# Kernel optimization log

Hardware: AMD Instinct MI355X
Metric: run time of the kernel (lower is better)

## Reference

```python
import jax, jax.numpy as jnp
import numpy as np
import math

B, S, DM, H = 2, 2048, 1024, 16
HD = DM // H  # head_dim = 64


def setup_inputs() -> dict:
    key = jax.random.key(0)
    ks = jax.random.split(key, 7)
    mk = lambda k, shp, s=1.0: jax.random.normal(k, shp, dtype=jnp.float32) * s
    return {
        "q": mk(ks[0], (B, S, DM)),
        "k": mk(ks[1], (B, S, DM)),
        "v": mk(ks[2], (B, S, DM)),
        "wq": mk(ks[3], (DM, DM), 0.02),
        "wk": mk(ks[4], (DM, DM), 0.02),
        "wv": mk(ks[5], (DM, DM), 0.02),
        "wo": mk(ks[6], (DM, DM), 0.02),
    }


def reference(q, k, v, wq, wk, wv, wo):
    bsz, seqlen, _ = q.shape
    # bias-free linear projections: y = x @ W.T (torch nn.Linear layout [out,in])
    def proj(x, w):
        y = jnp.einsum('bsd,ed->bse', x, w)
        return y.reshape(bsz, seqlen, H, HD).transpose(0, 2, 1, 3)  # (B,H,S,HD)
    xq, xk, xv = proj(q, wq), proj(k, wk), proj(v, wv)
    scores = jnp.einsum('bhqd,bhkd->bhqk', xq, xk) / math.sqrt(HD)  # (B,H,S,S)
    # causal mask: -inf above the diagonal
    causal = jnp.tril(jnp.ones((seqlen, seqlen), dtype=bool))
    scores = jnp.where(causal[None, None], scores, -jnp.inf)
    probs = jax.nn.softmax(scores.astype(jnp.float32), axis=-1).astype(xq.dtype)
    # dropout p=0.0 -> identity in eval / p=0 config
    out = jnp.einsum('bhqk,bhkd->bhqd', probs, xv)  # (B,H,S,HD)
    out = out.transpose(0, 2, 1, 3).reshape(bsz, seqlen, DM)
    return jnp.einsum('bsd,ed->bse', out, wo)
```

## Files before the change

kernel.cpp:

```cpp
#include <hip/hip_runtime.h>
#include <hip/hip_bf16.h>
#include <stdint.h>

#define NB 2
#define NS 2048
#define NDM 1024
#define NH 16
#define NHD 64
#define NTOK (NB * NS)

typedef __bf16 bf16x8 __attribute__((ext_vector_type(8)));
typedef float f32x4 __attribute__((ext_vector_type(4)));
typedef uint16_t u16x8 __attribute__((ext_vector_type(8)));

static __device__ __forceinline__ uint16_t f2bf(float f) {
  __bf16 b = (__bf16)f;
  union { __bf16 b; uint16_t u; } x; x.b = b;
  return x.u;
}

static __device__ __forceinline__ u16x8 cvt8(float4 a, float4 b) {
  u16x8 v;
  v[0] = f2bf(a.x); v[1] = f2bf(a.y); v[2] = f2bf(a.z); v[3] = f2bf(a.w);
  v[4] = f2bf(b.x); v[5] = f2bf(b.y); v[6] = f2bf(b.z); v[7] = f2bf(b.w);
  return v;
}

static __device__ __forceinline__ void gload_lds16(const void* g, void* l) {
  __builtin_amdgcn_global_load_lds(
      (const __attribute__((address_space(1))) void*)g,
      (__attribute__((address_space(3))) void*)l, 16, 0, 0);
}

__global__ __launch_bounds__(256) void cvt_w(
    const float* __restrict__ w0, const float* __restrict__ w1,
    const float* __restrict__ w2, const float* __restrict__ w3,
    uint16_t* __restrict__ o0, uint16_t* __restrict__ o1,
    uint16_t* __restrict__ o2, uint16_t* __restrict__ o3) {
  int y = blockIdx.y;
  const float* src = (y == 0) ? w0 : (y == 1) ? w1 : (y == 2) ? w2 : w3;
  uint16_t* dst = (y == 0) ? o0 : (y == 1) ? o1 : (y == 2) ? o2 : o3;
  int i = ((int)blockIdx.x * 256 + (int)threadIdx.x) * 8;
  float4 a = *(const float4*)(src + i);
  float4 b = *(const float4*)(src + i + 4);
  *(u16x8*)&dst[i] = cvt8(a, b);
}

__global__ __launch_bounds__(256) void cvt_x(
    const float* __restrict__ x0, const float* __restrict__ x1,
    const float* __restrict__ x2, uint16_t* __restrict__ o0,
    uint16_t* __restrict__ o1, uint16_t* __restrict__ o2) {
  int y = blockIdx.y;
  const float* src = (y == 0) ? x0 : (y == 1) ? x1 : x2;
  uint16_t* dst = (y == 0) ? o0 : (y == 1) ? o1 : o2;
  int i = ((int)blockIdx.x * 256 + (int)threadIdx.x) * 8;
  float4 a = *(const float4*)(src + i);
  float4 b = *(const float4*)(src + i + 4);
  *(u16x8*)&dst[i] = cvt8(a, b);
}

__global__ __launch_bounds__(256) void proj_gemm(
    const uint16_t* __restrict__ xbq, const uint16_t* __restrict__ xbk,
    const uint16_t* __restrict__ xbv, const uint16_t* __restrict__ wqb,
    const uint16_t* __restrict__ wkb, const uint16_t* __restrict__ wvb,
    uint16_t* __restrict__ XQ, uint16_t* __restrict__ XK,
    uint16_t* __restrict__ XVT) {
  __shared__ uint16_t SM[2][2][128][64];
  int z = blockIdx.z;
  const uint16_t* A = (z == 0) ? xbq : (z == 1) ? xbk : xbv;
  const uint16_t* W = (z == 0) ? wqb : (z == 1) ? wkb : wvb;
  int m0 = blockIdx.x * 128, n0 = blockIdx.y * 128;
  int tid = threadIdx.x;
  int lane = tid & 63, w = tid >> 6;
  int g = lane >> 4, r16 = lane & 15;
  int wm = w >> 1, wn = w & 1;
  int bce = ((lane & 7) ^ ((lane >> 3) & 7)) * 8;
  int brlane = lane >> 3;

  f32x4 acc[4][4] = {};

  #pragma unroll
  for (int i = 0; i < 4; ++i) {
    int row = w * 32 + i * 8;
    gload_lds16(A + (size_t)(m0 + row + brlane) * NDM + bce, &SM[0][0][row][0]);
    gload_lds16(W + (size_t)(n0 + row + brlane) * NDM + bce, &SM[0][1][row][0]);
  }
  __syncthreads();

  for (int t = 0; t < 16; ++t) {
    int cur = t & 1, nxt = cur ^ 1;
    if (t < 15) {
      int k1 = (t + 1) * 64;
      #pragma unroll
      for (int i = 0; i < 4; ++i) {
        int row = w * 32 + i * 8;
        gload_lds16(A + (size_t)(m0 + row + brlane) * NDM + k1 + bce,
                    &SM[nxt][0][row][0]);
        gload_lds16(W + (size_t)(n0 + row + brlane) * NDM + k1 + bce,
                    &SM[nxt][1][row][0]);
      }
    }

    #pragma unroll
    for (int kc = 0; kc < 2; ++kc) {
      bf16x8 af[4], bf[4];
      #pragma unroll
      for (int i = 0; i < 4; ++i) {
        int gran = (kc * 4 + g) ^ (r16 & 7);
        af[i] = *(const bf16x8*)&SM[cur][0][wm * 64 + i * 16 + r16][gran * 8];
        bf[i] = *(const bf16x8*)&SM[cur][1][wn * 64 + i * 16 + r16][gran * 8];
      }
      #pragma unroll
      for (int mi = 0; mi < 4; ++mi)
        #pragma unroll
        for (int ni = 0; ni < 4; ++ni)
          acc[mi][ni] = __builtin_amdgcn_mfma_f32_16x16x32_bf16(
              af[mi], bf[ni], acc[mi][ni], 0, 0, 0);
    }
    __syncthreads();
  }

  if (z == 2) {
    uint16_t* T = &SM[0][0][0][0];
    #pragma unroll
    for (int mi = 0; mi < 4; ++mi) {
      #pragma unroll
      for (int ni = 0; ni < 4; ++ni) {
        int tr = wn * 64 + ni * 16 + r16;
        int tc = wm * 64 + mi * 16 + g * 4;
        int gran = tc >> 3, sub = g & 1;
        f32x4 a = acc[mi][ni];
        ushort4 pk;
        pk.x = f2bf(a[0]); pk.y = f2bf(a[1]);
        pk.z = f2bf(a[2]); pk.w = f2bf(a[3]);
        *(ushort4*)(T + tr * 128 + ((gran ^ (tr & 7)) << 3) + (sub << 2)) = pk;
      }
    }
    __syncthreads();
    #pragma unroll
    for (int it = 0; it < 8; ++it) {
      int row = it * 16 + (tid >> 4);
      int grn = tid & 15;
      u16x8 vv = *(const u16x8*)(T + row * 128 + ((grn ^ (row & 7)) << 3));
      *(u16x8*)&XVT[(size_t)(n0 + row) * NTOK + m0 + grn * 8] = vv;
    }
  } else {
    float scale = (z == 0) ? 0.125f * 1.44269504088896340736f : 1.0f;
    uint16_t* Y = (z == 0) ? XQ : XK;
    #pragma unroll
    for (int mi = 0; mi < 4; ++mi) {
      #pragma unroll
      for (int ni = 0; ni < 4; ++ni) {
        int m = m0 + wm * 64 + mi * 16 + g * 4;
        int n = n0 + wn * 64 + ni * 16 + r16;
        f32x4 a = acc[mi][ni];
        #pragma unroll
        for (int j = 0; j < 4; ++j)
          Y[(size_t)(m + j) * NDM + n] = f2bf(a[j] * scale);
      }
    }
  }
}

__global__ __launch_bounds__(128) void attn_kernel(
    const uint16_t* __restrict__ XQ, const uint16_t* __restrict__ XK,
    const uint16_t* __restrict__ XVT, uint16_t* __restrict__ AO) {
  __shared__ uint16_t Klds[64][72];
  __shared__ uint16_t Vlds[64][72];
  __shared__ uint16_t Plds[2][16][72];

  int tid = threadIdx.x;
  int lane = tid & 63;
  int w = tid >> 6;
  int g = lane >> 4, r16 = lane & 15;
  int srow = tid >> 1;
  int scol = (tid & 1) * 32;

  int item = (int)blockIdx.x;
  int qc = 63 - (item >> 5);
  int bh = item & 31;
  int b = bh >> 4, h = bh & 15;
  int q0 = qc * 32;
  int q0w = q0 + w * 16;
  int T = (qc >> 1) + 1;

  const uint16_t* qb =
      XQ + (size_t)(b * NS + q0w + r16) * NDM + h * NHD + g * 8;
  bf16x8 qf0 = *(const bf16x8*)qb;
  bf16x8 qf1 = *(const bf16x8*)(qb + 32);

  f32x4 oacc[4] = {};
  float mrow = -1e30f, lsum = 0.f;

  const uint16_t* kbase = XK + (size_t)(b * NS + srow) * NDM + h * NHD + scol;
  const uint16_t* vbase = XVT + (size_t)(h * NHD + srow) * NTOK + b * NS + scol;

  u16x8 kr[4], vr[4];
  #pragma unroll
  for (int i = 0; i < 4; ++i) {
    kr[i] = *(const u16x8*)(kbase + i * 8);
    vr[i] = *(const u16x8*)(vbase + i * 8);
  }

  for (int t = 0; t < T; ++t) {
    int kv0 = t * 64;
    __syncthreads();
    #pragma unroll
    for (int i = 0; i < 4; ++i) {
      *(u16x8*)&Klds[srow][scol + i * 8] = kr[i];
      *(u16x8*)&Vlds[srow][scol + i * 8] = vr[i];
    }
    __syncthreads();
    if (t + 1 < T) {
      const uint16_t* kp = kbase + (size_t)(t + 1) * 64 * NDM;
      const uint16_t* vp = vbase + (t + 1) * 64;
      #pragma unroll
      for (int i = 0; i < 4; ++i) {
        kr[i] = *(const u16x8*)(kp + i * 8);
        vr[i] = *(const u16x8*)(vp + i * 8);
      }
    }

    f32x4 sc[4];
    __builtin_amdgcn_s_setprio(1);
    #pragma unroll
    for (int t4 = 0; t4 < 4; ++t4) {
      bf16x8 kf0 = *(const bf16x8*)&Klds[t4 * 16 + r16][g * 8];
      bf16x8 kf1 = *(const bf16x8*)&Klds[t4 * 16 + r16][32 + g * 8];
      f32x4 x = __builtin_amdgcn_mfma_f32_16x16x32_bf16(
          kf0, qf0, (f32x4){0.f, 0.f, 0.f, 0.f}, 0, 0, 0);
      x = __builtin_amdgcn_mfma_f32_16x16x32_bf16(kf1, qf1, x, 0, 0, 0);
      sc[t4] = x;
    }
    __builtin_amdgcn_s_setprio(0);

    #pragma unroll
    for (int t4 = 0; t4 < 4; ++t4) {
      if (kv0 + t4 * 16 + 15 > q0w) {
        #pragma unroll
        for (int j = 0; j < 4; ++j)
          if (kv0 + t4 * 16 + g * 4 + j > q0w + r16) sc[t4][j] = -1e30f;
      }
    }

    float m16 = fmaxf(
        fmaxf(fmaxf(fmaxf(sc[0][0], sc[0][1]), fmaxf(sc[0][2], sc[0][3])),
              fmaxf(fmaxf(sc[1][0], sc[1][1]), fmaxf(sc[1][2], sc[1][3]))),
        fmaxf(fmaxf(fmaxf(sc[2][0], sc[2][1]), fmaxf(sc[2][2], sc[2][3])),
              fmaxf(fmaxf(sc[3][0], sc[3][1]), fmaxf(sc[3][2], sc[3][3]))));
    m16 = fmaxf(m16, __shfl_xor(m16, 16));
    m16 = fmaxf(m16, __shfl_xor(m16, 32));

    if (!__all(m16 <= mrow + 8.0f)) {
      float mnew = fmaxf(mrow, m16);
      float sf = __builtin_amdgcn_exp2f(mrow - mnew);
      mrow = mnew;
      lsum *= sf;
      #pragma unroll
      for (int j = 0; j < 4; ++j) {
        float sfj = __shfl(sf, g * 4 + j);
        #pragma unroll
        for (int dt = 0; dt < 4; ++dt) oacc[dt][j] *= sfj;
      }
    }

    #pragma unroll
    for (int t4 = 0; t4 < 4; ++t4) {
      float p0 = __builtin_amdgcn_exp2f(sc[t4][0] - mrow);
      float p1 = __builtin_amdgcn_exp2f(sc[t4][1] - mrow);
      float p2 = __builtin_amdgcn_exp2f(sc[t4][2] - mrow);
      float p3 = __builtin_amdgcn_exp2f(sc[t4][3] - mrow);
      lsum += (p0 + p1) + (p2 + p3);
      ushort4 pk;
      pk.x = f2bf(p0); pk.y = f2bf(p1); pk.z = f2bf(p2); pk.w = f2bf(p3);
      *(ushort4*)&Plds[w][r16][t4 * 16 + g * 4] = pk;
    }

    bf16x8 pa0 = *(const bf16x8*)&Plds[w][r16][g * 8];
    bf16x8 pa1 = *(const bf16x8*)&Plds[w][r16][32 + g * 8];
    __builtin_amdgcn_s_setprio(1);
    #pragma unroll
    for (int dt = 0; dt < 4; ++dt) {
      bf16x8 vf0 = *(const bf16x8*)&Vlds[dt * 16 + r16][g * 8];
      bf16x8 vf1 = *(const bf16x8*)&Vlds[dt * 16 + r16][32 + g * 8];
      oacc[dt] = __builtin_amdgcn_mfma_f32_16x16x32_bf16(pa0, vf0, oacc[dt], 0, 0, 0);
      oacc[dt] = __builtin_amdgcn_mfma_f32_16x16x32_bf16(pa1, vf1, oacc[dt], 0, 0, 0);
    }
    __builtin_amdgcn_s_setprio(0);
  }

  float l2 = lsum + __shfl_xor(lsum, 16);
  float ltot = l2 + __shfl_xor(l2, 32);
  #pragma unroll
  for (int j = 0; j < 4; ++j) {
    float lt = __shfl(ltot, g * 4 + j);
    float inv = 1.0f / lt;
    size_t ro = (size_t)(b * NS + q0 + w * 16 + g * 4 + j) * NDM + h * NHD;
    #pragma unroll
    for (int dt = 0; dt < 4; ++dt)
      AO[ro + dt * 16 + r16] = f2bf(oacc[dt][j] * inv);
  }
}

__global__ __launch_bounds__(256) void out_gemm(
    const uint16_t* __restrict__ AO, const uint16_t* __restrict__ wob,
    float* __restrict__ out) {
  __shared__ uint16_t As[2][128][64];
  __shared__ uint16_t Bs[2][128][64];
  int m0 = blockIdx.x * 128, n0 = blockIdx.y * 128;
  int tid = threadIdx.x;
  int lane = tid & 63, w = tid >> 6;
  int g = lane >> 4, r16 = lane & 15;
  int wm = w >> 1, wn = w & 1;
  int bce = ((lane & 7) ^ ((lane >> 3) & 7)) * 8;
  int brlane = lane >> 3;

  f32x4 acc[4][4] = {};

  #pragma unroll
  for (int i = 0; i < 4; ++i) {
    int row = w * 32 + i * 8;
    gload_lds16(AO + (size_t)(m0 + row + brlane) * NDM + bce, &As[0][row][0]);
    gload_lds16(wob + (size_t)(n0 + row + brlane) * NDM + bce, &Bs[0][row][0]);
  }
  __syncthreads();

  for (int t = 0; t < 16; ++t) {
    int cur = t & 1, nxt = cur ^ 1;
    if (t < 15) {
      int k1 = (t + 1) * 64;
      #pragma unroll
      for (int i = 0; i < 4; ++i) {
        int row = w * 32 + i * 8;
        gload_lds16(AO + (size_t)(m0 + row + brlane) * NDM + k1 + bce,
                    &As[nxt][row][0]);
        gload_lds16(wob + (size_t)(n0 + row + brlane) * NDM + k1 + bce,
                    &Bs[nxt][row][0]);
      }
    }

    #pragma unroll
    for (int kc = 0; kc < 2; ++kc) {
      bf16x8 af[4], bf[4];
      #pragma unroll
      for (int i = 0; i < 4; ++i) {
        int gran = (kc * 4 + g) ^ (r16 & 7);
        af[i] = *(const bf16x8*)&As[cur][wm * 64 + i * 16 + r16][gran * 8];
        bf[i] = *(const bf16x8*)&Bs[cur][wn * 64 + i * 16 + r16][gran * 8];
      }
      #pragma unroll
      for (int mi = 0; mi < 4; ++mi)
        #pragma unroll
        for (int ni = 0; ni < 4; ++ni)
          acc[mi][ni] = __builtin_amdgcn_mfma_f32_16x16x32_bf16(
              af[mi], bf[ni], acc[mi][ni], 0, 0, 0);
    }
    __syncthreads();
  }

  #pragma unroll
  for (int mi = 0; mi < 4; ++mi) {
    #pragma unroll
    for (int ni = 0; ni < 4; ++ni) {
      int m = m0 + wm * 64 + mi * 16 + g * 4;
      int n = n0 + wn * 64 + ni * 16 + r16;
      #pragma unroll
      for (int j = 0; j < 4; ++j)
        out[(size_t)(m + j) * NDM + n] = acc[mi][ni][j];
    }
  }
}

extern "C" void kernel_launch(void* const* d_in, const int* in_sizes, int n_in,
                              void* d_out, int out_size, void* d_ws,
                              size_t ws_size, hipStream_t stream) {
  const float* q  = (const float*)d_in[0];
  const float* k  = (const float*)d_in[1];
  const float* v  = (const float*)d_in[2];
  const float* wq = (const float*)d_in[3];
  const float* wk = (const float*)d_in[4];
  const float* wv = (const float*)d_in[5];
  const float* wo = (const float*)d_in[6];

  const size_t XN = (size_t)NTOK * NDM;
  const size_t WN = (size_t)NDM * NDM;
  uint16_t* XQ  = (uint16_t*)d_ws;
  uint16_t* XK  = XQ + XN;
  uint16_t* XVT = XK + XN;
  uint16_t* WQB = XVT + XN;
  uint16_t* WKB = WQB + WN;
  uint16_t* WVB = WKB + WN;
  uint16_t* WOB = WVB + WN;
  uint16_t* XBQ = WOB + WN;
  uint16_t* XBK = XBQ + XN;
  uint16_t* XBV = XBK + XN;
  uint16_t* AO  = XBQ;

  cvt_w<<<dim3(WN / (256 * 8), 4), 256, 0, stream>>>(
      wq, wk, wv, wo, WQB, WKB, WVB, WOB);
  cvt_x<<<dim3(XN / (256 * 8), 3), 256, 0, stream>>>(
      q, k, v, XBQ, XBK, XBV);
  proj_gemm<<<dim3(NTOK / 128, NDM / 128, 3), 256, 0, stream>>>(
      XBQ, XBK, XBV, WQB, WKB, WVB, XQ, XK, XVT);
  attn_kernel<<<dim3(2048), 128, 0, stream>>>(XQ, XK, XVT, AO);
  out_gemm<<<dim3(NTOK / 128, NDM / 128), 256, 0, stream>>>(
      AO, WOB, (float*)d_out);
}
```

Measured before the change: 118.6 us.

## Enlarge attention query tile to 64 rows with async double-buffered K/V loads

The attention kernel now handles 64 query rows per block, two 16-row sub-tiles per wave, so each K/V tile staged in LDS feeds twice as many MFMAs, and the grid is halved. K/V loads switch from register staging plus LDS stores to direct global-to-LDS loads into double buffers with an XOR swizzle. This drops one barrier per iteration and lets the next tile's fetch overlap compute. Block-to-work mapping is also reordered in a serpentine pattern across heads. It costs more registers, fewer blocks for load balance on the causal triangle, and a bit more wasted masked work on diagonal tiles.

```diff
diff --git a/kernel.cpp b/kernel.cpp
--- a/kernel.cpp
+++ b/kernel.cpp
@@ -165,140 +165,166 @@
 __global__ __launch_bounds__(128) void attn_kernel(
     const uint16_t* __restrict__ XQ, const uint16_t* __restrict__ XK,
     const uint16_t* __restrict__ XVT, uint16_t* __restrict__ AO) {
-  __shared__ uint16_t Klds[64][72];
-  __shared__ uint16_t Vlds[64][72];
-  __shared__ uint16_t Plds[2][16][72];
+  __shared__ uint16_t Klds[2][64][64];
+  __shared__ uint16_t Vlds[2][64][64];
+  __shared__ uint16_t Plds[2][16][68];
 
   int tid = threadIdx.x;
   int lane = tid & 63;
   int w = tid >> 6;
   int g = lane >> 4, r16 = lane & 15;
-  int srow = tid >> 1;
-  int scol = (tid & 1) * 32;
-
-  int item = (int)blockIdx.x;
-  int qc = 63 - (item >> 5);
-  int bh = item & 31;
+  int swz = r16 & 7;
+
+  int bid = (int)blockIdx.x;
+  int v = bid >> 5;
+  int rr = v >> 3, uu = v & 7;
+  int qc = rr * 8 + ((rr & 1) ? (7 - uu) : uu);
+  int bh = (bid & 7) * 4 + ((bid >> 3) & 3);
   int b = bh >> 4, h = bh & 15;
-  int q0 = qc * 32;
-  int q0w = q0 + w * 16;
-  int T = (qc >> 1) + 1;
-
-  const uint16_t* qb =
-      XQ + (size_t)(b * NS + q0w + r16) * NDM + h * NHD + g * 8;
-  bf16x8 qf0 = *(const bf16x8*)qb;
-  bf16x8 qf1 = *(const bf16x8*)(qb + 32);
-
-  f32x4 oacc[4] = {};
-  float mrow = -1e30f, lsum = 0.f;
-
-  const uint16_t* kbase = XK + (size_t)(b * NS + srow) * NDM + h * NHD + scol;
-  const uint16_t* vbase = XVT + (size_t)(h * NHD + srow) * NTOK + b * NS + scol;
-
-  u16x8 kr[4], vr[4];
+  int q0 = qc * 64;
+  int T = qc + 1;
+
+  bf16x8 qf[2][2];
   #pragma unroll
-  for (int i = 0; i < 4; ++i) {
-    kr[i] = *(const u16x8*)(kbase + i * 8);
-    vr[i] = *(const u16x8*)(vbase + i * 8);
-  }
-
+  for (int s = 0; s < 2; ++s) {
+    const uint16_t* qb =
+        XQ + (size_t)(b * NS + q0 + w * 32 + s * 16 + r16) * NDM + h * NHD + g * 8;
+    qf[s][0] = *(const bf16x8*)qb;
+    qf[s][1] = *(const bf16x8*)(qb + 32);
+  }
+
+  f32x4 oacc[2][4] = {};
+  float mrow[2] = {-1e30f, -1e30f};
+  float lsum[2] = {0.f, 0.f};
+
+  int bce = ((lane & 7) ^ (lane >> 3)) * 8;
+  int srl = lane >> 3;
+  const uint16_t* kstg = XK + (size_t)(b * NS + srl) * NDM + h * NHD + bce;
+  const uint16_t* vstg = XVT + (size_t)(h * NHD + srl) * NTOK + b * NS + bce;
+
+  if (w == 0) {
+    #pragma unroll
+    for (int i = 0; i < 8; ++i)
+      gload_lds16(kstg + (size_t)(i * 8) * NDM, &Klds[0][i * 8][0]);
+  } else {
+    #pragma unroll
+    for (int i = 0; i < 8; ++i)
+      gload_lds16(vstg + (size_t)(i * 8) * NTOK, &Vlds[0][i * 8][0]);
+  }
+
+  int cur = 0;
   for (int t = 0; t < T; ++t) {
     int kv0 = t * 64;
     __syncthreads();
-    #pragma unroll
-    for (int i = 0; i < 4; ++i) {
-      *(u16x8*)&Klds[srow][scol + i * 8] = kr[i];
-      *(u16x8*)&Vlds[srow][scol + i * 8] = vr[i];
-    }
-    __syncthreads();
     if (t + 1 < T) {
-      const uint16_t* kp = kbase + (size_t)(t + 1) * 64 * NDM;
-      const uint16_t* vp = vbase + (t + 1) * 64;
-      #pragma unroll
-      for (int i = 0; i < 4; ++i) {
-        kr[i] = *(const u16x8*)(kp + i * 8);
-        vr[i] = *(const u16x8*)(vp + i * 8);
-      }
-    }
-
-    f32x4 sc[4];
+      int kv1 = kv0 + 64;
+      if (w == 0) {
+        #pragma unroll
+        for (int i = 0; i < 8; ++i)
+          gload_lds16(kstg + (size_t)(kv1 + i * 8) * NDM, &Klds[cur ^ 1][i * 8][0]);
+      } else {
+        #pragma unroll
+        for (int i = 0; i < 8; ++i)
+          gload_lds16(vstg + kv1 + (size_t)(i * 8) * NTOK, &Vlds[cur ^ 1][i * 8][0]);
+      }
+    }
+
+    f32x4 sc[2][4];
     __builtin_amdgcn_s_setprio(1);
     #pragma unroll
     for (int t4 = 0; t4 < 4; ++t4) {
-      bf16x8 kf0 = *(const bf16x8*)&Klds[t4 * 16 + r16][g * 8];
-      bf16x8 kf1 = *(const bf16x8*)&Klds[t4 * 16 + r16][32 + g * 8];
-      f32x4 x = __builtin_amdgcn_mfma_f32_16x16x32_bf16(
-          kf0, qf0, (f32x4){0.f, 0.f, 0.f, 0.f}, 0, 0, 0);
-      x = __builtin_amdgcn_mfma_f32_16x16x32_bf16(kf1, qf1, x, 0, 0, 0);
-      sc[t4] = x;
+      bf16x8 kf0 = *(const bf16x8*)&Klds[cur][t4 * 16 + r16][(g ^ swz) * 8];
+      bf16x8 kf1 = *(const bf16x8*)&Klds[cur][t4 * 16 + r16][((g + 4) ^ swz) * 8];
+      #pragma unroll
+      for (int s = 0; s < 2; ++s) {
+        f32x4 x = __builtin_amdgcn_mfma_f32_16x16x32_bf16(
+            kf0, qf[s][0], (f32x4){0.f, 0.f, 0.f, 0.f}, 0, 0, 0);
+        x = __builtin_amdgcn_mfma_f32_16x16x32_bf16(kf1, qf[s][1], x, 0, 0, 0);
+        sc[s][t4] = x;
+      }
     }
     __builtin_amdgcn_s_setprio(0);
 
-    #pragma unroll
-    for (int t4 = 0; t4 < 4; ++t4) {
-      if (kv0 + t4 * 16 + 15 > q0w) {
-        #pragma unroll
-        for (int j = 0; j < 4; ++j)
-          if (kv0 + t4 * 16 + g * 4 + j > q0w + r16) sc[t4][j] = -1e30f;
-      }
-    }
-
-    float m16 = fmaxf(
-        fmaxf(fmaxf(fmaxf(sc[0][0], sc[0][1]), fmaxf(sc[0][2], sc[0][3])),
-              fmaxf(fmaxf(sc[1][0], sc[1][1]), fmaxf(sc[1][2], sc[1][3]))),
-        fmaxf(fmaxf(fmaxf(sc[2][0], sc[2][1]), fmaxf(sc[2][2], sc[2][3])),
-              fmaxf(fmaxf(sc[3][0], sc[3][1]), fmaxf(sc[3][2], sc[3][3]))));
-    m16 = fmaxf(m16, __shfl_xor(m16, 16));
-    m16 = fmaxf(m16, __shfl_xor(m16, 32));
-
-    if (!__all(m16 <= mrow + 8.0f)) {
-      float mnew = fmaxf(mrow, m16);
-      float sf = __builtin_amdgcn_exp2f(mrow - mnew);
-      mrow = mnew;
-      lsum *= sf;
-      #pragma unroll
-      for (int j = 0; j < 4; ++j) {
-        float sfj = __shfl(sf, g * 4 + j);
-        #pragma unroll
-        for (int dt = 0; dt < 4; ++dt) oacc[dt][j] *= sfj;
-      }
-    }
-
-    #pragma unroll
-    for (int t4 = 0; t4 < 4; ++t4) {
-      float p0 = __builtin_amdgcn_exp2f(sc[t4][0] - mrow);
-      float p1 = __builtin_amdgcn_exp2f(sc[t4][1] - mrow);
-      float p2 = __builtin_amdgcn_exp2f(sc[t4][2] - mrow);
-      float p3 = __builtin_amdgcn_exp2f(sc[t4][3] - mrow);
-      lsum += (p0 + p1) + (p2 + p3);
-      ushort4 pk;
-      pk.x = f2bf(p0); pk.y = f2bf(p1); pk.z = f2bf(p2); pk.w = f2bf(p3);
-      *(ushort4*)&Plds[w][r16][t4 * 16 + g * 4] = pk;
-    }
-
-    bf16x8 pa0 = *(const bf16x8*)&Plds[w][r16][g * 8];
-    bf16x8 pa1 = *(const bf16x8*)&Plds[w][r16][32 + g * 8];
+    bf16x8 pa[2][2];
+    #pragma unroll
+    for (int s = 0; s < 2; ++s) {
+      int q0w = q0 + w * 32 + s * 16;
+      #pragma unroll
+      for (int t4 = 0; t4 < 4; ++t4) {
+        if (kv0 + t4 * 16 + 15 > q0w) {
+          #pragma unroll
+          for (int j = 0; j < 4; ++j)
+            if (kv0 + t4 * 16 + g * 4 + j > q0w + r16) sc[s][t4][j] = -1e30f;
+        }
+      }
+
+      float m16 = fmaxf(
+          fmaxf(fmaxf(fmaxf(sc[s][0][0], sc[s][0][1]), fmaxf(sc[s][0][2], sc[s][0][3])),
+                fmaxf(fmaxf(sc[s][1][0], sc[s][1][1]), fmaxf(sc[s][1][2], sc[s][1][3]))),
+          fmaxf(fmaxf(fmaxf(sc[s][2][0], sc[s][2][1]), fmaxf(sc[s][2][2], sc[s][2][3])),
+                fmaxf(fmaxf(sc[s][3][0], sc[s][3][1]), fmaxf(sc[s][3][2], sc[s][3][3]))));
+      m16 = fmaxf(m16, __shfl_xor(m16, 16));
+      m16 = fmaxf(m16, __shfl_xor(m16, 32));
+
+      if (!__all(m16 <= mrow[s] + 8.0f)) {
+        float mnew = fmaxf(mrow[s], m16);
+        float sf = __builtin_amdgcn_exp2f(mrow[s] - mnew);
+        mrow[s] = mnew;
+        lsum[s] *= sf;
+        #pragma unroll
+        for (int j = 0; j < 4; ++j) {
+          float sfj = __shfl(sf, g * 4 + j);
+          #pragma unroll
+          for (int dt = 0; dt < 4; ++dt) oacc[s][dt][j] *= sfj;
+        }
+      }
+
+      #pragma unroll
+      for (int t4 = 0; t4 < 4; ++t4) {
+        float p0 = __builtin_amdgcn_exp2f(sc[s][t4][0] - mrow[s]);
+        float p1 = __builtin_amdgcn_exp2f(sc[s][t4][1] - mrow[s]);
+        float p2 = __builtin_amdgcn_exp2f(sc[s][t4][2] - mrow[s]);
+        float p3 = __builtin_amdgcn_exp2f(sc[s][t4][3] - mrow[s]);
+        lsum[s] += (p0 + p1) + (p2 + p3);
+        ushort4 pk;
+        pk.x = f2bf(p0); pk.y = f2bf(p1); pk.z = f2bf(p2); pk.w = f2bf(p3);
+        *(ushort4*)&Plds[w][r16][t4 * 16 + g * 4] = pk;
+      }
+      pa[s][0] = *(const bf16x8*)&Plds[w][r16][g * 8];
+      pa[s][1] = *(const bf16x8*)&Plds[w][r16][32 + g * 8];
+    }
+
     __builtin_amdgcn_s_setprio(1);
     #pragma unroll
     for (int dt = 0; dt < 4; ++dt) {
-      bf16x8 vf0 = *(const bf16x8*)&Vlds[dt * 16 + r16][g * 8];
-      bf16x8 vf1 = *(const bf16x8*)&Vlds[dt * 16 + r16][32 + g * 8];
-      oacc[dt] = __builtin_amdgcn_mfma_f32_16x16x32_bf16(pa0, vf0, oacc[dt], 0, 0, 0);
-      oacc[dt] = __builtin_amdgcn_mfma_f32_16x16x32_bf16(pa1, vf1, oacc[dt], 0, 0, 0);
+      bf16x8 vf0 = *(const bf16x8*)&Vlds[cur][dt * 16 + r16][(g ^ swz) * 8];
+      bf16x8 vf1 = *(const bf16x8*)&Vlds[cur][dt * 16 + r16][((g + 4) ^ swz) * 8];
+      #pragma unroll
+      for (int s = 0; s < 2; ++s) {
+        oacc[s][dt] = __builtin_amdgcn_mfma_f32_16x16x32_bf16(
+            pa[s][0], vf0, oacc[s][dt], 0, 0, 0);
+        oacc[s][dt] = __builtin_amdgcn_mfma_f32_16x16x32_bf16(
+            pa[s][1], vf1, oacc[s][dt], 0, 0, 0);
+      }
     }
     __builtin_amdgcn_s_setprio(0);
-  }
-
-  float l2 = lsum + __shfl_xor(lsum, 16);
-  float ltot = l2 + __shfl_xor(l2, 32);
+    cur ^= 1;
+  }
+
   #pragma unroll
-  for (int j = 0; j < 4; ++j) {
-    float lt = __shfl(ltot, g * 4 + j);
-    float inv = 1.0f / lt;
-    size_t ro = (size_t)(b * NS + q0 + w * 16 + g * 4 + j) * NDM + h * NHD;
-    #pragma unroll
-    for (int dt = 0; dt < 4; ++dt)
-      AO[ro + dt * 16 + r16] = f2bf(oacc[dt][j] * inv);
+  for (int s = 0; s < 2; ++s) {
+    float l2 = lsum[s] + __shfl_xor(lsum[s], 16);
+    float ltot = l2 + __shfl_xor(l2, 32);
+    #pragma unroll
+    for (int j = 0; j < 4; ++j) {
+      float lt = __shfl(ltot, g * 4 + j);
+      float inv = 1.0f / lt;
+      size_t ro =
+          (size_t)(b * NS + q0 + w * 32 + s * 16 + g * 4 + j) * NDM + h * NHD;
+      #pragma unroll
+      for (int dt = 0; dt < 4; ++dt)
+        AO[ro + dt * 16 + r16] = f2bf(oacc[s][dt][j] * inv);
+    }
   }
 }
 
@@ -402,7 +428,7 @@
       q, k, v, XBQ, XBK, XBV);
   proj_gemm<<<dim3(NTOK / 128, NDM / 128, 3), 256, 0, stream>>>(
       XBQ, XBK, XBV, WQB, WKB, WVB, XQ, XK, XVT);
-  attn_kernel<<<dim3(2048), 128, 0, stream>>>(XQ, XK, XVT, AO);
+  attn_kernel<<<dim3(1024), 128, 0, stream>>>(XQ, XK, XVT, AO);
   out_gemm<<<dim3(NTOK / 128, NDM / 128), 256, 0, stream>>>(
       AO, WOB, (float*)d_out);
 }
```

Result: slower. 133.6 us (+12.6%).
